# Kernel tuning notes

Hardware: AMD Instinct MI355X
Metric: run time of the kernel (lower is better)

## Reference

```python
import jax, jax.numpy as jnp
import numpy as np

B, N, E = 16, 512, 6144          # graphs, sites/graph, edges/graph
D = 256                          # embed_dimension
RBF_DIM = 128
M = 6                            # num_messages
MAXZ = 84                        # max_atomic_num
INIT_MAX_DIST, INIT_GAP = 7.0, 30.0


def setup_inputs() -> dict:
    key = jax.random.key(0)
    ks = jax.random.split(key, 20)
    s = 0.02
    inp = {
        "site_class": jax.random.randint(ks[0], (B, N), 0, MAXZ, dtype=jnp.int64),
        "distance": jax.random.uniform(ks[1], (B, E), dtype=jnp.float32) * INIT_MAX_DIST,
        "connectivity": jax.random.randint(ks[2], (B, E, 2), 0, N, dtype=jnp.int64),
        # learned parameters
        "atom_emb": jax.random.normal(ks[3], (MAXZ, D), jnp.float32) * s,
        "mean_emb": jnp.zeros((MAXZ, 1), jnp.float32),  # Constant(output_bias=0.0)
        "centers": jnp.arange(RBF_DIM, dtype=jnp.float32) * (INIT_MAX_DIST / RBF_DIM),
        "gap": jnp.float32(INIT_GAP),
        "bond_W": jax.random.normal(ks[4], (RBF_DIM, D), jnp.float32) * s,
        "bond_b": jnp.zeros((D,), jnp.float32),
        "offset_W": jax.random.normal(ks[5], (D, 1), jnp.float32) * 1e-6,
        "offset_b": jnp.zeros((1,), jnp.float32),
        # per-message EdgeUpdate ConcatDense: Dense(2D, relu) -> Dense(D), input 3D
        "edge_W1": jax.random.normal(ks[6], (M, 3 * D, 2 * D), jnp.float32) * s,
        "edge_b1": jnp.zeros((M, 2 * D), jnp.float32),
        "edge_W2": jax.random.normal(ks[7], (M, 2 * D, D), jnp.float32) * s,
        "edge_b2": jnp.zeros((M, D), jnp.float32),
        # per-message NodeUpdate ConcatDense: input 2D
        "node_W1": jax.random.normal(ks[8], (M, 2 * D, 2 * D), jnp.float32) * s,
        "node_b1": jnp.zeros((M, 2 * D), jnp.float32),
        "node_W2": jax.random.normal(ks[9], (M, 2 * D, D), jnp.float32) * s,
        "node_b2": jnp.zeros((M, D), jnp.float32),
    }
    return inp


def _gather(x, idx):
    # x: [B, N, D], idx: [B, E] -> [B, E, D]
    return x[jnp.arange(x.shape[0])[:, None], idx]


def reference(site_class, distance, connectivity,
              atom_emb, mean_emb, centers, gap, bond_W, bond_b,
              offset_W, offset_b,
              edge_W1, edge_b1, edge_W2, edge_b2,
              node_W1, node_b1, node_W2, node_b2):
    atom_mask = site_class != 0                     # [B, N] (Embedding mask_zero)
    bond_mask = distance != 0.0                     # [B, E] (RBFExpansion mask)

    atom_state = atom_emb[site_class]               # [B, N, D]
    atom_mean = mean_emb[site_class]                # [B, N, 1]

    # RBF expansion: exp(-gap * (d - centers)^2), masked distances -> 1.0
    d = distance[..., None]
    d = jnp.where(d != 0.0, d, 1.0)
    rbf = jnp.exp(-((d - centers) ** 2) * gap)      # [B, E, RBF_DIM]
    bond_state = rbf @ bond_W + bond_b              # [B, E, D]

    bidx = jnp.arange(site_class.shape[0])[:, None]
    idx0 = connectivity[..., 0]                     # scatter target
    idx1 = connectivity[..., 1]                     # message source

    n_msg = edge_W1.shape[0]
    for i in range(n_msg):
        # EdgeUpdate: concat(bond, src_atom, tgt_atom) -> Dense(2D, relu) -> Dense(D)
        src = _gather(atom_state, idx1)
        tgt = _gather(atom_state, idx0)
        h = jnp.concatenate([bond_state, src, tgt], axis=-1)      # [B, E, 3D]
        h = jax.nn.relu(h @ edge_W1[i] + edge_b1[i])
        h = h @ edge_W2[i] + edge_b2[i]
        h = jnp.where(bond_mask[..., None], h, 0.0)
        bond_state = bond_state + h

        # NodeUpdate: concat(src_atom, bond) -> MLP -> segment-sum onto idx0
        src = _gather(atom_state, idx1)
        m = jnp.concatenate([src, bond_state], axis=-1)           # [B, E, 2D]
        m = jax.nn.relu(m @ node_W1[i] + node_b1[i])
        m = m @ node_W2[i] + node_b2[i]
        new_atom = jnp.zeros_like(atom_state).at[bidx, idx0].add(m)
        new_atom = jnp.where(atom_mask[..., None], new_atom, 0.0)
        atom_state = atom_state + new_atom

    atom_mean = atom_mean + (atom_state @ offset_W + offset_b)   # [B, N, 1]

    # masked global average pooling over sites
    mask_f = atom_mask[..., None].astype(atom_mean.dtype)
    pooled = jnp.sum(atom_mean * mask_f, axis=1) / jnp.sum(mask_f, axis=1)
    return pooled  # [B, 1]
```

## Files before the change

kernel.cpp:

```cpp
#include <hip/hip_runtime.h>
#include <hip/hip_bf16.h>
#include <stdint.h>
#include <stddef.h>

#define Bb 16
#define Nn 512
#define Ee 6144
#define Dd 256
#define ROWS (Bb * Ee)

typedef short bf16x8 __attribute__((ext_vector_type(8)));
typedef float f32x4 __attribute__((ext_vector_type(4)));

__device__ __forceinline__ unsigned short f2bf(float f) {
  union { float f; unsigned u; } v; v.f = f;
  return (unsigned short)((v.u + 0x7fffu + ((v.u >> 16) & 1u)) >> 16);
}
__device__ __forceinline__ float bf2f(unsigned short h) {
  union { unsigned u; float f; } v; v.u = ((unsigned)h) << 16;
  return v.f;
}

__device__ __forceinline__ void gload16(const void* g, void* l) {
  __builtin_amdgcn_global_load_lds(
      (const __attribute__((address_space(1))) void*)g,
      (__attribute__((address_space(3))) void*)l, 16, 0, 0);
}

__global__ void transpose_w(const float* __restrict__ in, unsigned short* __restrict__ out,
                            int K, int Ncol) {
  __shared__ float tile[32][33];
  const float* inb = in + (size_t)blockIdx.z * K * Ncol;
  unsigned short* outb = out + (size_t)blockIdx.z * K * Ncol;
  int bk = blockIdx.x * 32, bn = blockIdx.y * 32;
  int tx = threadIdx.x, ty = threadIdx.y;
#pragma unroll
  for (int i = 0; i < 32; i += 8)
    tile[ty + i][tx] = inb[(size_t)(bk + ty + i) * Ncol + (bn + tx)];
  __syncthreads();
#pragma unroll
  for (int i = 0; i < 32; i += 8)
    outb[(size_t)(bn + ty + i) * K + (bk + tx)] = f2bf(tile[tx][ty + i]);
}

__global__ void atom_init(const int* __restrict__ cls, const float* __restrict__ emb,
                          float* __restrict__ atom, unsigned short* __restrict__ atomBf) {
  int s_ = blockIdx.x, d = threadIdx.x;
  size_t o = (size_t)s_ * Dd + d;
  float v = emb[(size_t)cls[s_] * Dd + d];
  atom[o] = v;
  atomBf[o] = f2bf(v);
}

__global__ void atom_fix(const int* __restrict__ cls, const float* __restrict__ emb,
                         float* __restrict__ atom, unsigned short* __restrict__ atomBf) {
  int s_ = blockIdx.x, d = threadIdx.x;
  size_t o = (size_t)s_ * Dd + d;
  float v = (cls[s_] == 0) ? emb[d] : atom[o];
  atom[o] = v;
  atomBf[o] = f2bf(v);
}

__global__ __launch_bounds__(256, 2) void gemm_rbf(
    const unsigned short* __restrict__ Wt, const float* __restrict__ bias,
    const float* __restrict__ dist, const float* __restrict__ centers,
    const float* __restrict__ gapP, unsigned short* __restrict__ bondHi,
    unsigned short* __restrict__ bondLo) {
  __shared__ __align__(16) unsigned short lA[128 * 64];
  __shared__ __align__(16) unsigned short lB[128 * 64];
  const int t = threadIdx.x;
  const int bm = blockIdx.x * 128, bn = blockIdx.y * 128;
  const int srow = t & 127, skc = (t >> 7) * 32;
  const int m = bm + srow;
  float dval = dist[m]; if (dval == 0.f) dval = 1.f;
  float gapv = *gapP;
  const unsigned short* pBt = Wt + (size_t)(bn + srow) * 128 + skc;
  const int wid = t >> 6, lane = t & 63;
  const int wm = (wid & 1) * 64, wn = (wid >> 1) * 64;
  const int fr = lane & 15, fk0 = (lane >> 4) * 8;
  f32x4 acc[4][4] = {};
  for (int k0 = 0; k0 < 128; k0 += 64) {
    union __align__(16) { unsigned short us[32]; bf16x8 v[4]; } ab, bb;
#pragma unroll
    for (int j = 0; j < 32; j++) {
      float x = dval - centers[k0 + skc + j];
      ab.us[j] = f2bf(__expf(-gapv * x * x));
    }
    const bf16x8* s = (const bf16x8*)(pBt + k0);
#pragma unroll
    for (int c = 0; c < 4; c++) bb.v[c] = s[c];
    __syncthreads();
#pragma unroll
    for (int c = 0; c < 4; c++) {
      int byteo = (skc + c * 8) * 2;
      int swz = byteo ^ ((srow & 7) << 4);
      *(bf16x8*)((char*)lA + srow * 128 + swz) = ab.v[c];
      *(bf16x8*)((char*)lB + srow * 128 + swz) = bb.v[c];
    }
    __syncthreads();
#pragma unroll
    for (int kk = 0; kk < 64; kk += 32) {
      bf16x8 af[4], bfq[4];
#pragma unroll
      for (int f = 0; f < 4; f++) {
        int r = wm + f * 16 + fr;
        af[f] = *(const bf16x8*)((const char*)lA + r * 128 + (((kk + fk0) * 2) ^ ((r & 7) << 4)));
        int cq = wn + f * 16 + fr;
        bfq[f] = *(const bf16x8*)((const char*)lB + cq * 128 + (((kk + fk0) * 2) ^ ((cq & 7) << 4)));
      }
#pragma unroll
      for (int i = 0; i < 4; i++)
#pragma unroll
        for (int j = 0; j < 4; j++)
          acc[i][j] = __builtin_amdgcn_mfma_f32_16x16x32_bf16(af[i], bfq[j], acc[i][j], 0, 0, 0);
    }
  }
#pragma unroll
  for (int i = 0; i < 4; i++)
#pragma unroll
    for (int j = 0; j < 4; j++) {
      int gcol = bn + wn + j * 16 + fr;
      float bvv = bias[gcol];
#pragma unroll
      for (int v = 0; v < 4; v++) {
        int grow = bm + wm + i * 16 + (lane >> 4) * 4 + v;
        float val = acc[i][j][v] + bvv;
        size_t o = (size_t)grow * Dd + gcol;
        unsigned short hi = f2bf(val);
        bondHi[o] = hi;
        bondLo[o] = f2bf(val - bf2f(hi));
      }
    }
}

struct GP {
  const unsigned short* Wt;
  const float* bias;
  const unsigned short* bondHi;
  unsigned short* bondLo;
  const unsigned short* atomBf;
  const unsigned short* h1;
  const int* conn;
  const float* dist;
  unsigned short* outH1;
  unsigned short* outBondHi;
  float* atomMaster;
};

#define A_EDGE1 0
#define A_NODE1 1
#define A_H1    2
#define EP_H1RELU 0
#define EP_EDGE2  1
#define EP_NODE2  2

template <int K, int NC, int AL, int EP>
__global__ __launch_bounds__(512, 2) void gemm256(GP p) {
  __shared__ __align__(16) char lds[131072];
  const int t = threadIdx.x;
  const int w = t >> 6, l = t & 63;
  constexpr int NT = NC / 256;

  const int nwg = gridDim.x;
  const int q8 = nwg >> 3;
  const int sb = (blockIdx.x & 7) * q8 + (blockIdx.x >> 3);
  const int bn = (sb % NT) * 256;
  const int bm = (sb / NT) * 256;

  const unsigned swz = (unsigned)(((l & 7) ^ (l >> 3)) << 4);

  unsigned offA0[4], offA1[4], offA2[4], offB[4];
#pragma unroll
  for (int i = 0; i < 4; i++) {
    int rA = i * 64 + w * 8 + (l >> 3);
    if (AL == A_H1) {
      offA0[i] = (unsigned)(bm + rA) * (K * 2) + swz;
      offA1[i] = offA0[i]; offA2[i] = offA0[i];
    } else {
      int gr = bm + rA;
      int b = gr / Ee;
      int i0 = p.conn[2 * gr], i1 = p.conn[2 * gr + 1];
      unsigned bondOff = (unsigned)gr * 512u + swz;
      unsigned srcOff  = (unsigned)(b * Nn + i1) * 512u + swz;
      unsigned tgtOff  = (unsigned)(b * Nn + i0) * 512u + swz;
      if (AL == A_EDGE1) { offA0[i] = bondOff; offA1[i] = srcOff; offA2[i] = tgtOff; }
      else               { offA0[i] = srcOff;  offA1[i] = bondOff; offA2[i] = bondOff; }
    }
    offB[i] = (unsigned)(bn + rA) * (K * 2) + swz;
  }

  const int fr = l & 15;
  const int q4 = l >> 4;
  const int wm = (w >> 2) * 128;
  const int wn = (w & 3) * 64;

  f32x4 acc[8][4] = {};

  auto stage = [&](int buf, int k0) {
#pragma unroll
    for (int i = 0; i < 4; i++) {
      const char* src;
      if (AL == A_H1) {
        src = (const char*)p.h1 + (offA0[i] + (unsigned)k0 * 2);
      } else if (AL == A_EDGE1) {
        int s = k0 >> 8;
        src = (s == 0 ? (const char*)p.bondHi + offA0[i]
                      : (const char*)p.atomBf + (s == 1 ? offA1[i] : offA2[i]))
              + (k0 & 255) * 2;
      } else {
        src = (k0 < 256 ? (const char*)p.atomBf + offA0[i]
                        : (const char*)p.bondHi + offA1[i])
              + (k0 & 255) * 2;
      }
      gload16(src, lds + buf * 32768 + i * 8192 + w * 1024);
      gload16((const char*)p.Wt + offB[i] + (unsigned)k0 * 2,
              lds + 65536 + buf * 32768 + i * 8192 + w * 1024);
    }
  };

  auto compute = [&](int buf) {
#pragma unroll
    for (int kk = 0; kk < 2; kk++) {
      const int ck = kk * 4 + q4;
      bf16x8 av[8], bv[4];
#pragma unroll
      for (int f = 0; f < 8; f++) {
        int r = wm + f * 16 + fr;
        av[f] = *(const bf16x8*)(lds + buf * 32768 + r * 128 + ((ck ^ (r & 7)) << 4));
      }
#pragma unroll
      for (int n = 0; n < 4; n++) {
        int rq = wn + n * 16 + fr;
        bv[n] = *(const bf16x8*)(lds + 65536 + buf * 32768 + rq * 128 + ((ck ^ (rq & 7)) << 4));
      }
      __builtin_amdgcn_s_setprio(1);
#pragma unroll
      for (int f = 0; f < 8; f++)
#pragma unroll
        for (int n = 0; n < 4; n++)
          acc[f][n] = __builtin_amdgcn_mfma_f32_16x16x32_bf16(av[f], bv[n], acc[f][n], 0, 0, 0);
      __builtin_amdgcn_s_setprio(0);
    }
  };

  constexpr int nT = K / 64;
  stage(0, 0);
  stage(1, 64);

  for (int tt = 0; tt < nT; tt++) {
    asm volatile("s_waitcnt vmcnt(8)" ::: "memory");
    __builtin_amdgcn_s_barrier();
    __builtin_amdgcn_sched_barrier(0);
    compute(tt & 1);
    __builtin_amdgcn_s_barrier();
    __builtin_amdgcn_sched_barrier(0);
    if (tt + 2 < nT) stage(tt & 1, (tt + 2) * 64);
  }

  float bias4[4];
#pragma unroll
  for (int n = 0; n < 4; n++) bias4[n] = p.bias[bn + wn + n * 16 + fr];

#pragma unroll
  for (int f = 0; f < 8; f++) {
#pragma unroll
    for (int v = 0; v < 4; v++) {
      int grow = bm + wm + f * 16 + q4 * 4 + v;
      if (EP == EP_H1RELU) {
#pragma unroll
        for (int n = 0; n < 4; n++) {
          int gcol = bn + wn + n * 16 + fr;
          float val = acc[f][n][v] + bias4[n];
          p.outH1[(size_t)grow * 512 + gcol] = f2bf(fmaxf(val, 0.f));
        }
      } else if (EP == EP_EDGE2) {
        if (p.dist[grow] != 0.f) {
#pragma unroll
          for (int n = 0; n < 4; n++) {
            int gcol = bn + wn + n * 16 + fr;
            size_t o = (size_t)grow * Dd + gcol;
            float cur = bf2f(p.bondHi[o]) + bf2f(p.bondLo[o]);
            float nv = cur + acc[f][n][v] + bias4[n];
            unsigned short hi = f2bf(nv);
            p.outBondHi[o] = hi;
            p.bondLo[o] = f2bf(nv - bf2f(hi));
          }
        }
      } else {
        int b = grow / Ee;
        int tg = p.conn[2 * grow];
        float* dst = p.atomMaster + ((size_t)b * Nn + tg) * Dd;
#pragma unroll
        for (int n = 0; n < 4; n++) {
          int gcol = bn + wn + n * 16 + fr;
          atomicAdd(dst + gcol, acc[f][n][v] + bias4[n]);
        }
      }
    }
  }
}

__global__ void pool_k(const float* __restrict__ atom, const int* __restrict__ cls,
                       const float* __restrict__ meanEmb, const float* __restrict__ oW,
                       const float* __restrict__ ob, float* __restrict__ out) {
  __shared__ float w[Dd];
  __shared__ float red[256];
  __shared__ float redc[256];
  int b = blockIdx.x, t = threadIdx.x;
  w[t] = oW[t];
  __syncthreads();
  float sum = 0.f, cnt = 0.f;
  for (int n = t; n < Nn; n += 256) {
    int site = b * Nn + n;
    int c = cls[site];
    const float* a = atom + (size_t)site * Dd;
    float dot = 0.f;
    for (int d = 0; d < Dd; d++) dot += a[d] * w[d];
    if (c != 0) { sum += meanEmb[c] + dot + ob[0]; cnt += 1.f; }
  }
  red[t] = sum; redc[t] = cnt;
  __syncthreads();
  for (int s = 128; s > 0; s >>= 1) {
    if (t < s) { red[t] += red[t + s]; redc[t] += redc[t + s]; }
    __syncthreads();
  }
  if (t == 0) out[b] = red[0] / redc[0];
}

extern "C" void kernel_launch(void* const* d_in, const int* in_sizes, int n_in,
                              void* d_out, int out_size, void* d_ws, size_t ws_size,
                              hipStream_t stream) {
  const int* site_class = (const int*)d_in[0];
  const float* distance = (const float*)d_in[1];
  const int* conn       = (const int*)d_in[2];
  const float* atom_emb = (const float*)d_in[3];
  const float* mean_emb = (const float*)d_in[4];
  const float* centers  = (const float*)d_in[5];
  const float* gapP     = (const float*)d_in[6];
  const float* bond_W   = (const float*)d_in[7];
  const float* bond_b   = (const float*)d_in[8];
  const float* offset_W = (const float*)d_in[9];
  const float* offset_b = (const float*)d_in[10];
  const float* edge_W1  = (const float*)d_in[11];
  const float* edge_b1  = (const float*)d_in[12];
  const float* edge_W2  = (const float*)d_in[13];
  const float* edge_b2  = (const float*)d_in[14];
  const float* node_W1  = (const float*)d_in[15];
  const float* node_b1  = (const float*)d_in[16];
  const float* node_W2  = (const float*)d_in[17];
  const float* node_b2  = (const float*)d_in[18];

  char* ws = (char*)d_ws;
  float* atom            = (float*)(ws + 0);
  unsigned short* atomBf = (unsigned short*)(ws + 8388608);
  unsigned short* bondHi = (unsigned short*)(ws + 12582912);
  unsigned short* bondLo = (unsigned short*)(ws + 62914560);
  unsigned short* h1     = (unsigned short*)(ws + 113246208);
  unsigned short* bWT    = (unsigned short*)(ws + 213909504);
  unsigned short* eW1T   = (unsigned short*)(ws + 213975040);
  unsigned short* eW2T   = (unsigned short*)(ws + 218693632);
  unsigned short* nW1T   = (unsigned short*)(ws + 220266496);
  unsigned short* nW2T   = (unsigned short*)(ws + 223412224);

  dim3 tb(32, 8);
  transpose_w<<<dim3(4, 8, 1), tb, 0, stream>>>(bond_W, bWT, 128, 256);
  transpose_w<<<dim3(24, 16, 6), tb, 0, stream>>>(edge_W1, eW1T, 768, 512);
  transpose_w<<<dim3(16, 8, 6), tb, 0, stream>>>(edge_W2, eW2T, 512, 256);
  transpose_w<<<dim3(16, 16, 6), tb, 0, stream>>>(node_W1, nW1T, 512, 512);
  transpose_w<<<dim3(16, 8, 6), tb, 0, stream>>>(node_W2, nW2T, 512, 256);

  atom_init<<<Bb * Nn, 256, 0, stream>>>(site_class, atom_emb, atom, atomBf);
  gemm_rbf<<<dim3(768, 2), 256, 0, stream>>>(bWT, bond_b, distance, centers, gapP, bondHi, bondLo);

  GP base{};
  base.conn = conn; base.dist = distance;
  base.bondHi = bondHi; base.bondLo = bondLo; base.atomBf = atomBf; base.h1 = h1;
  base.outH1 = h1; base.outBondHi = bondHi; base.atomMaster = atom;

  for (int i = 0; i < 6; i++) {
    {
      GP q = base;
      q.Wt = eW1T + (size_t)i * 512 * 768; q.bias = edge_b1 + i * 512;
      gemm256<768, 512, A_EDGE1, EP_H1RELU><<<768, 512, 0, stream>>>(q);
    }
    {
      GP q = base;
      q.Wt = eW2T + (size_t)i * 256 * 512; q.bias = edge_b2 + i * 256;
      gemm256<512, 256, A_H1, EP_EDGE2><<<384, 512, 0, stream>>>(q);
    }
    {
      GP q = base;
      q.Wt = nW1T + (size_t)i * 512 * 512; q.bias = node_b1 + i * 512;
      gemm256<512, 512, A_NODE1, EP_H1RELU><<<768, 512, 0, stream>>>(q);
    }
    {
      GP q = base;
      q.Wt = nW2T + (size_t)i * 256 * 512; q.bias = node_b2 + i * 256;
      gemm256<512, 256, A_H1, EP_NODE2><<<384, 512, 0, stream>>>(q);
    }
    atom_fix<<<Bb * Nn, 256, 0, stream>>>(site_class, atom_emb, atom, atomBf);
  }

  pool_k<<<Bb, 256, 0, stream>>>(atom, site_class, mean_emb, offset_W, offset_b, (float*)d_out);
}
```

Before: 2.343 ms.

## Switch GEMM main loop to 4-slot K=32 pipeline with one barrier per step

The GEMM K-loop now uses 32-wide K slices in a 4-slot ring buffer with three tiles in flight, replacing the previous 2-buffer 64-wide scheme. Each iteration issues the next stage load before computing and uses a single barrier instead of two. LDS row pitch and the swizzle are changed to match 64-byte rows. The aim is deeper latency hiding and less synchronization, at the cost of smaller MFMA batches per barrier and more loop iterations.

```diff
diff --git a/kernel.cpp b/kernel.cpp
--- a/kernel.cpp
+++ b/kernel.cpp
@@ -162,101 +162,105 @@
   constexpr int NT = NC / 256;
 
   const int nwg = gridDim.x;
-  const int q8 = nwg >> 3;
-  const int sb = (blockIdx.x & 7) * q8 + (blockIdx.x >> 3);
+  const int q8v = nwg >> 3;
+  const int sb = (blockIdx.x & 7) * q8v + (blockIdx.x >> 3);
   const int bn = (sb % NT) * 256;
   const int bm = (sb / NT) * 256;
 
-  const unsigned swz = (unsigned)(((l & 7) ^ (l >> 3)) << 4);
-
-  unsigned offA0[4], offA1[4], offA2[4], offB[4];
-#pragma unroll
-  for (int i = 0; i < 4; i++) {
-    int rA = i * 64 + w * 8 + (l >> 3);
+  unsigned offA0[2], offA1[2], offA2[2], offB[2];
+#pragma unroll
+  for (int h = 0; h < 2; h++) {
+    int row = h * 128 + w * 16 + (l >> 2);
+    unsigned swz = (unsigned)(((l & 3) ^ ((row >> 1) & 3)) << 4);
     if (AL == A_H1) {
-      offA0[i] = (unsigned)(bm + rA) * (K * 2) + swz;
-      offA1[i] = offA0[i]; offA2[i] = offA0[i];
+      offA0[h] = (unsigned)(bm + row) * (K * 2) + swz;
+      offA1[h] = offA0[h]; offA2[h] = offA0[h];
     } else {
-      int gr = bm + rA;
+      int gr = bm + row;
       int b = gr / Ee;
       int i0 = p.conn[2 * gr], i1 = p.conn[2 * gr + 1];
       unsigned bondOff = (unsigned)gr * 512u + swz;
       unsigned srcOff  = (unsigned)(b * Nn + i1) * 512u + swz;
       unsigned tgtOff  = (unsigned)(b * Nn + i0) * 512u + swz;
-      if (AL == A_EDGE1) { offA0[i] = bondOff; offA1[i] = srcOff; offA2[i] = tgtOff; }
-      else               { offA0[i] = srcOff;  offA1[i] = bondOff; offA2[i] = bondOff; }
-    }
-    offB[i] = (unsigned)(bn + rA) * (K * 2) + swz;
+      if (AL == A_EDGE1) { offA0[h] = bondOff; offA1[h] = srcOff; offA2[h] = tgtOff; }
+      else               { offA0[h] = srcOff;  offA1[h] = bondOff; offA2[h] = bondOff; }
+    }
+    offB[h] = (unsigned)(bn + row) * (K * 2) + swz;
   }
 
   const int fr = l & 15;
   const int q4 = l >> 4;
-  const int wm = (w >> 2) * 128;
-  const int wn = (w & 3) * 64;
+  const int wr = w >> 2;
+  const int wc = w & 3;
 
   f32x4 acc[8][4] = {};
 
-  auto stage = [&](int buf, int k0) {
-#pragma unroll
-    for (int i = 0; i < 4; i++) {
-      const char* src;
+  auto stage = [&](int T2) {
+    const int k0 = T2 * 32;
+    const int sl = T2 & 3;
+#pragma unroll
+    for (int h = 0; h < 2; h++) {
+      const char* srcA;
       if (AL == A_H1) {
-        src = (const char*)p.h1 + (offA0[i] + (unsigned)k0 * 2);
+        srcA = (const char*)p.h1 + offA0[h] + (unsigned)k0 * 2;
       } else if (AL == A_EDGE1) {
         int s = k0 >> 8;
-        src = (s == 0 ? (const char*)p.bondHi + offA0[i]
-                      : (const char*)p.atomBf + (s == 1 ? offA1[i] : offA2[i]))
-              + (k0 & 255) * 2;
+        srcA = (s == 0 ? (const char*)p.bondHi + offA0[h]
+                       : (const char*)p.atomBf + (s == 1 ? offA1[h] : offA2[h]))
+               + (k0 & 255) * 2;
       } else {
-        src = (k0 < 256 ? (const char*)p.atomBf + offA0[i]
-                        : (const char*)p.bondHi + offA1[i])
-              + (k0 & 255) * 2;
+        srcA = (k0 < 256 ? (const char*)p.atomBf + offA0[h]
+                         : (const char*)p.bondHi + offA1[h]) + (k0 & 255) * 2;
       }
-      gload16(src, lds + buf * 32768 + i * 8192 + w * 1024);
-      gload16((const char*)p.Wt + offB[i] + (unsigned)k0 * 2,
-              lds + 65536 + buf * 32768 + i * 8192 + w * 1024);
+      char* dst = lds + sl * 16384 + h * 8192 + w * 1024;
+      gload16(srcA, dst);
+      gload16((const char*)p.Wt + offB[h] + (unsigned)k0 * 2, dst + 65536);
     }
   };
 
-  auto compute = [&](int buf) {
-#pragma unroll
-    for (int kk = 0; kk < 2; kk++) {
-      const int ck = kk * 4 + q4;
-      bf16x8 av[8], bv[4];
-#pragma unroll
-      for (int f = 0; f < 8; f++) {
-        int r = wm + f * 16 + fr;
-        av[f] = *(const bf16x8*)(lds + buf * 32768 + r * 128 + ((ck ^ (r & 7)) << 4));
-      }
-#pragma unroll
-      for (int n = 0; n < 4; n++) {
-        int rq = wn + n * 16 + fr;
-        bv[n] = *(const bf16x8*)(lds + 65536 + buf * 32768 + rq * 128 + ((ck ^ (rq & 7)) << 4));
-      }
-      __builtin_amdgcn_s_setprio(1);
-#pragma unroll
-      for (int f = 0; f < 8; f++)
-#pragma unroll
-        for (int n = 0; n < 4; n++)
-          acc[f][n] = __builtin_amdgcn_mfma_f32_16x16x32_bf16(av[f], bv[n], acc[f][n], 0, 0, 0);
-      __builtin_amdgcn_s_setprio(0);
-    }
+  auto compute = [&](int sl) {
+    const char* Ab = lds + sl * 16384;
+    const char* Bp = lds + 65536 + sl * 16384;
+    bf16x8 av[8], bv[4];
+#pragma unroll
+    for (int f = 0; f < 8; f++) {
+      int r = wr * 128 + f * 16 + fr;
+      av[f] = *(const bf16x8*)(Ab + r * 64 + ((q4 ^ ((r >> 1) & 3)) << 4));
+    }
+#pragma unroll
+    for (int n = 0; n < 4; n++) {
+      int rq = wc * 64 + n * 16 + fr;
+      bv[n] = *(const bf16x8*)(Bp + rq * 64 + ((q4 ^ ((rq >> 1) & 3)) << 4));
+    }
+    __builtin_amdgcn_s_setprio(1);
+#pragma unroll
+    for (int f = 0; f < 8; f++)
+#pragma unroll
+      for (int n = 0; n < 4; n++)
+        acc[f][n] = __builtin_amdgcn_mfma_f32_16x16x32_bf16(av[f], bv[n], acc[f][n], 0, 0, 0);
+    __builtin_amdgcn_s_setprio(0);
   };
 
-  constexpr int nT = K / 64;
-  stage(0, 0);
-  stage(1, 64);
-
-  for (int tt = 0; tt < nT; tt++) {
+  constexpr int nT = K / 32;
+  stage(0); stage(1); stage(2);
+
+  for (int tt = 0; tt < nT - 2; ++tt) {
     asm volatile("s_waitcnt vmcnt(8)" ::: "memory");
     __builtin_amdgcn_s_barrier();
     __builtin_amdgcn_sched_barrier(0);
-    compute(tt & 1);
-    __builtin_amdgcn_s_barrier();
-    __builtin_amdgcn_sched_barrier(0);
-    if (tt + 2 < nT) stage(tt & 1, (tt + 2) * 64);
-  }
-
+    if (tt + 3 < nT) stage(tt + 3);
+    compute(tt & 3);
+  }
+  asm volatile("s_waitcnt vmcnt(4)" ::: "memory");
+  __builtin_amdgcn_s_barrier();
+  __builtin_amdgcn_sched_barrier(0);
+  compute((nT - 2) & 3);
+  asm volatile("s_waitcnt vmcnt(0)" ::: "memory");
+  __builtin_amdgcn_s_barrier();
+  __builtin_amdgcn_sched_barrier(0);
+  compute((nT - 1) & 3);
+
+  const int wm = wr * 128, wn = wc * 64;
   float bias4[4];
 #pragma unroll
   for (int n = 0; n < 4; n++) bias4[n] = p.bias[bn + wn + n * 16 + fr];
```

After: 2.376 ms. Within noise of the previous version (+1.4%).
